# Performance work log

Measured on AMD Instinct MI355X. Metric: run time of the kernel, lower is better.

## Reference

```python
import jax, jax.numpy as jnp
import numpy as np

V = 23
EDGES = [(2,1),(3,1),(6,12),(6,10),(6,8),(8,10),(7,13),(7,11),(7,9),(9,11),(2,4),(4,6),(3,5),(5,7),(2,3),(2,14),(3,15),(14,15),(14,16),(15,17),(16,18),(17,19),(18,20),(18,22),(20,22),(19,21),(19,23),(21,23)]
K, H, C, OUT_C = 3, 8, 128, 128
N, T = 32, 256
BN_EPS = 1e-5


def _hop_matrix():
    # binarized union of I, Fw, Bw as in Graph.get_hop_distance
    A = np.zeros((V, V))
    for i, j in EDGES:
        A[i - 1, j - 1] = 1.0
        A[j - 1, i - 1] = 1.0
    np.fill_diagonal(A, 1.0)
    hop = np.full((V, V), V, dtype=np.int32)
    P = np.eye(V)
    for d in range(V):
        reach = P > 0
        hop = np.where(reach & (hop == V), d, hop)  # smallest d with reachability
        P = P @ A
    assert hop.max() < V, 'graph must be connected'
    return hop


def setup_inputs() -> dict:
    key = jax.random.key(0)
    ks = jax.random.split(key, 8)
    hop = _hop_matrix()  # (V,V) int32, max hop = 8 for mediapipe layout
    n_hop = int(hop.max()) + 1
    cin_g = C // H            # 16 in-channels per group
    cout_g = OUT_C // H       # 16 out-channels per group
    return {
        'x': jax.random.normal(ks[0], (N, C, T, V), dtype=jnp.float32),
        'emb_table': jax.random.normal(ks[1], (K, H, n_hop), dtype=jnp.float32) * 0.1,
        'A': jnp.tile(jnp.eye(V, dtype=jnp.float32)[None, None], (K, H, 1, 1))
             + 0.01 * jax.random.normal(ks[2], (K, H, V, V), dtype=jnp.float32),
        'conv_w': jax.random.normal(ks[3], (K * OUT_C, cin_g), dtype=jnp.float32) * 0.05,
        'conv_b': jax.random.normal(ks[4], (K * OUT_C,), dtype=jnp.float32) * 0.05,
        'bn_gamma': jax.random.uniform(ks[5], (OUT_C,), dtype=jnp.float32, minval=0.5, maxval=1.5),
        'bn_beta': jax.random.normal(ks[6], (OUT_C,), dtype=jnp.float32) * 0.1,
        'bn_mean': jax.random.normal(ks[7], (OUT_C,), dtype=jnp.float32) * 0.1,
        'bn_var': jax.random.uniform(jax.random.fold_in(key, 99), (OUT_C,), dtype=jnp.float32, minval=0.5, maxval=1.5),
        'hop': jnp.asarray(hop),
    }


def reference(x, emb_table, A, conv_w, conv_b, bn_gamma, bn_beta, bn_mean, bn_var, hop):
    n, c, t, v = x.shape
    k, h = A.shape[0], A.shape[1]
    cin_g = c // h
    # per-kernel/per-head learned adjacency from hop embedding table
    B = emb_table[:, :, hop]                                   # (k,h,v,v)
    def l2(w):
        return jnp.sqrt(jnp.sum(w * w, axis=-2, keepdims=True)) + 1e-4
    BnA = B / l2(B) + A / l2(A)                                # (k,h,v,v)
    xh = x.reshape(n, h, cin_g, t, v)
    # graph mixing over nodes (k-dim broadcast of x)
    y = jnp.einsum('nhctv,khvw->nkhctw', xh, BnA)              # (n,k,h,c/h,t,v)
    # grouped 1x1 conv (groups = k*h): per (k,h) group 16->16 channel mix
    w = conv_w.reshape(k, h, -1, cin_g)                        # (k,h,out/h,c/h)
    b = conv_b.reshape(k, h, -1)                               # (k,h,out/h)
    y = jnp.einsum('nkhctv,khoc->nkhotv', y, w) + b[None, :, :, :, None, None]
    y = y.reshape(n, k, -1, t, v).sum(axis=1)                  # (n,out_c,t,v)
    # BatchNorm2d (eval mode)
    inv = bn_gamma / jnp.sqrt(bn_var + BN_EPS)
    y = y * inv[None, :, None, None] + (bn_beta - bn_mean * inv)[None, :, None, None]
    # residual is identity (in_channels == out_channels)
    return jax.nn.relu(y + x)
```

## Files before the change

### kernel.cpp

```cpp
#include <hip/hip_runtime.h>
#include <hip/hip_bf16.h>
#include <stdint.h>

#define V 23
#define VP 24
#define KK 3
#define H 8
#define CG 16
#define TDIM 256
#define NB 32
#define TT 64
#define OUTC 128
#define CIN 128
#define KDIM 384
#define NSTEP 12
#define NCT 24
#define XROW 392

#define WS_BNA   0
#define WS_SCALE (KK*H*VP*VP)
#define WS_OFFS  (WS_SCALE + OUTC)
#define WS_WT    (WS_OFFS + OUTC)
#define WS_MB    (WS_WT + KK*H*CG*CG)
#define MB_ELEMS ((size_t)H * NSTEP * NCT * 512)
#define WS_NEED_BYTES ((size_t)WS_MB * 4 + MB_ELEMS * 2)
#define WS_SMALL_BYTES ((size_t)WS_MB * 4)

typedef __attribute__((ext_vector_type(8))) short bf16x8;
typedef __attribute__((ext_vector_type(4))) float f32x4;

static __device__ __forceinline__ uint32_t f2bf_rne(float f) {
  uint32_t u = __float_as_uint(f);
  return (u + 0x7fffu + ((u >> 16) & 1u)) >> 16;
}
static __device__ __forceinline__ float bf2f(uint16_t h) {
  return __uint_as_float(((uint32_t)h) << 16);
}

__global__ void prep1_kernel(const float* __restrict__ emb,
                             const float* __restrict__ A,
                             const float* __restrict__ conv_w,
                             const float* __restrict__ conv_b,
                             const float* __restrict__ gamma,
                             const float* __restrict__ beta,
                             const float* __restrict__ mean,
                             const float* __restrict__ var,
                             const int* __restrict__ hop,
                             int n_hop, float* __restrict__ ws) {
  int b = blockIdx.x;
  int tid = threadIdx.x;
  if (b < KK * H) {
    int w = tid;
    if (w >= 32) return;
    const float* e = emb + b * n_hop;
    const float* a = A + b * V * V;
    float nb = 1.f, na = 1.f;
    if (w < V) {
      float sb = 0.f, sa = 0.f;
      for (int v = 0; v < V; ++v) {
        float bv = e[hop[v * V + w]];
        float av = a[v * V + w];
        sb += bv * bv;
        sa += av * av;
      }
      nb = sqrtf(sb) + 1e-4f;
      na = sqrtf(sa) + 1e-4f;
    }
    float* dst = ws + WS_BNA + b * VP * VP;
    if (w < VP) {
      for (int v = 0; v < VP; ++v) {
        float val = 0.f;
        if (v < V && w < V)
          val = e[hop[v * V + w]] / nb + a[v * V + w] / na;
        dst[v * VP + w] = val;
      }
    }
  } else if (b == KK * H) {
    if (tid < OUTC) {
      float inv = gamma[tid] * rsqrtf(var[tid] + 1e-5f);
      float sb = conv_b[tid] + conv_b[OUTC + tid] + conv_b[2 * OUTC + tid];
      ws[WS_SCALE + tid] = inv;
      ws[WS_OFFS + tid] = beta[tid] - mean[tid] * inv + sb * inv;
    }
  } else {
    int idx = (b - KK * H - 1) * 256 + tid;
    if (idx < KK * H * CG * CG) {
      int o = idx & 15, c = (idx >> 4) & 15, h = (idx >> 8) & 7, k = idx >> 11;
      ws[WS_WT + ((k * H + h) * CG + c) * CG + o] =
          conv_w[((k * OUTC) + h * CG + o) * CG + c];
    }
  }
}

__global__ void prep2_kernel(float* __restrict__ ws) {
  int b = blockIdx.x;
  int h = b / NSTEP, s = b % NSTEP;
  uint16_t* mb = (uint16_t*)(ws + WS_MB);
  const float* wt = ws + WS_WT;
  const float* bna = ws + WS_BNA;
  for (int e = threadIdx.x; e < NCT * 64 * 8; e += 256) {
    int j = e & 7, lane = (e >> 3) & 63, ct = e >> 9;
    int k = s * 32 + ((lane >> 4) << 3) + j;
    int ci = k / VP, v = k % VP;
    int col = ct * 16 + (lane & 15);
    int o = col / VP, w = col - o * VP;
    float val = 0.f;
    if (v < V && w < V) {
      for (int kk = 0; kk < KK; ++kk)
        val += wt[((kk * H + h) * CG + ci) * CG + o] *
               bna[((kk * H + h) * VP + v) * VP + w];
    }
    mb[((size_t)(h * NSTEP + s) * NCT + ct) * 512 + lane * 8 + j] =
        (uint16_t)f2bf_rne(val);
  }
}

__global__ __launch_bounds__(256, 3) void gcn_main_mfma(
    const float* __restrict__ x,
    const float* __restrict__ ws,
    float* __restrict__ out) {
  __shared__ __align__(16) uint16_t Xa[TT * XROW];

  const int tid = threadIdx.x;
  const int t0 = blockIdx.x * TT;
  const int h  = blockIdx.y;
  const int n  = blockIdx.z;

  for (int u = tid; u < CG * TT * 6; u += 256) {
    int c = u / (TT * 6);
    int r = u % (TT * 6);
    int tt = r / 6, vc = r % 6;
    const float* xrow =
        x + ((size_t)((n * CIN + h * CG + c) * TDIM) + (t0 + tt)) * V;
    float f0 = xrow[vc * 4 + 0];
    float f1 = xrow[vc * 4 + 1];
    float f2 = xrow[vc * 4 + 2];
    float f3 = (vc < 5) ? xrow[vc * 4 + 3] : 0.f;
    uint32_t lo = f2bf_rne(f0) | (f2bf_rne(f1) << 16);
    uint32_t hi = f2bf_rne(f2) | (f2bf_rne(f3) << 16);
    *(uint2*)&Xa[tt * XROW + c * VP + vc * 4] = make_uint2(lo, hi);
  }
  __syncthreads();

  const int wave = tid >> 6, lane = tid & 63;
  const int m = lane & 15, q = lane >> 4;

  const uint16_t* mb = (const uint16_t*)(ws + WS_MB) +
                       ((size_t)h * NSTEP * NCT + wave * 6) * 512 + lane * 8;

  f32x4 acc[4][6];
#pragma unroll
  for (int rt = 0; rt < 4; ++rt)
#pragma unroll
    for (int c6 = 0; c6 < 6; ++c6) acc[rt][c6] = (f32x4){0.f, 0.f, 0.f, 0.f};

  for (int s = 0; s < NSTEP; ++s) {
    bf16x8 bf[6];
#pragma unroll
    for (int c6 = 0; c6 < 6; ++c6)
      bf[c6] = *(const bf16x8*)(mb + (size_t)(s * NCT + c6) * 512);
    bf16x8 af[4];
#pragma unroll
    for (int rt = 0; rt < 4; ++rt)
      af[rt] = *(const bf16x8*)&Xa[(rt * 16 + m) * XROW + s * 32 + q * 8];
#pragma unroll
    for (int c6 = 0; c6 < 6; ++c6)
#pragma unroll
      for (int rt = 0; rt < 4; ++rt)
        acc[rt][c6] = __builtin_amdgcn_mfma_f32_16x16x32_bf16(
            af[rt], bf[c6], acc[rt][c6], 0, 0, 0);
  }

#pragma unroll
  for (int c6 = 0; c6 < 6; ++c6) {
    int col = (wave * 6 + c6) * 16 + m;
    int o = col / VP, w = col - o * VP;
    float sc = ws[WS_SCALE + h * CG + o];
    float of = ws[WS_OFFS + h * CG + o];
    bool valid = (w < V);
    float* obase =
        out + ((size_t)(n * OUTC + h * CG + o) * TDIM + t0) * V + w;
#pragma unroll
    for (int rt = 0; rt < 4; ++rt) {
#pragma unroll
      for (int reg = 0; reg < 4; ++reg) {
        int row = rt * 16 + q * 4 + reg;
        float resid = bf2f(Xa[row * XROW + col]);
        float y = fmaf(acc[rt][c6][reg], sc, of) + resid;
        if (valid) obase[(size_t)row * V] = fmaxf(y, 0.f);
      }
    }
  }
}

__global__ __launch_bounds__(256, 3) void gcn_main_valu(
    const float* __restrict__ x,
    const float* __restrict__ ws,
    float* __restrict__ out) {
  __shared__ __align__(16) uint16_t Xs[CG * TT * VP];

  const int tid = threadIdx.x;
  const int t0 = blockIdx.x * TT;
  const int h  = blockIdx.y;
  const int n  = blockIdx.z;

  for (int u = tid; u < CG * TT * 6; u += 256) {
    int c = u / (TT * 6);
    int r = u % (TT * 6);
    int tt = r / 6, vc = r % 6;
    const float* xrow =
        x + ((size_t)((n * CIN + h * CG + c) * TDIM) + (t0 + tt)) * V;
    float f0 = xrow[vc * 4 + 0];
    float f1 = xrow[vc * 4 + 1];
    float f2 = xrow[vc * 4 + 2];
    float f3 = (vc < 5) ? xrow[vc * 4 + 3] : 0.f;
    uint32_t lo = f2bf_rne(f0) | (f2bf_rne(f1) << 16);
    uint32_t hi = f2bf_rne(f2) | (f2bf_rne(f3) << 16);
    *(uint2*)&Xs[(c * TT + tt) * VP + vc * 4] = make_uint2(lo, hi);
  }
  __syncthreads();

  const int oq = __builtin_amdgcn_readfirstlane(tid >> 6);
  const int tt = tid & 63;

  const float* wt  = ws + WS_WT  + ((size_t)h * CG * CG);
  const float* bna = ws + WS_BNA + ((size_t)h * VP * VP);

  float acc[4][VP];
#pragma unroll
  for (int o = 0; o < 4; ++o)
#pragma unroll
    for (int w = 0; w < VP; ++w) acc[o][w] = 0.f;

  for (int k = 0; k < KK; ++k) {
    const float* wtk  = wt  + (size_t)k * H * CG * CG;
    const float* bnak = bna + (size_t)k * H * VP * VP;
    for (int vb = 0; vb < 3; ++vb) {
      float xwv[4][8];
#pragma unroll
      for (int o = 0; o < 4; ++o)
#pragma unroll
        for (int j = 0; j < 8; ++j) xwv[o][j] = 0.f;
#pragma unroll 4
      for (int c = 0; c < CG; ++c) {
        uint4 raw = *(const uint4*)&Xs[(c * TT + tt) * VP + vb * 8];
        float4 wv = *(const float4*)&wtk[c * CG + (oq << 2)];
        float xv[8];
        xv[0] = __uint_as_float(raw.x << 16);
        xv[1] = __uint_as_float(raw.x & 0xffff0000u);
        xv[2] = __uint_as_float(raw.y << 16);
        xv[3] = __uint_as_float(raw.y & 0xffff0000u);
        xv[4] = __uint_as_float(raw.z << 16);
        xv[5] = __uint_as_float(raw.z & 0xffff0000u);
        xv[6] = __uint_as_float(raw.w << 16);
        xv[7] = __uint_as_float(raw.w & 0xffff0000u);
#pragma unroll
        for (int o = 0; o < 4; ++o) {
          float wo = (&wv.x)[o];
#pragma unroll
          for (int j = 0; j < 8; ++j) xwv[o][j] = fmaf(wo, xv[j], xwv[o][j]);
        }
      }
#pragma unroll
      for (int j = 0; j < 8; ++j) {
        const int v = vb * 8 + j;
        const float* bnrow = &bnak[v * VP];
#pragma unroll
        for (int wb = 0; wb < 6; ++wb) {
          float4 bn = *(const float4*)(bnrow + wb * 4);
#pragma unroll
          for (int o = 0; o < 4; ++o) {
            acc[o][wb * 4 + 0] = fmaf(xwv[o][j], bn.x, acc[o][wb * 4 + 0]);
            acc[o][wb * 4 + 1] = fmaf(xwv[o][j], bn.y, acc[o][wb * 4 + 1]);
            acc[o][wb * 4 + 2] = fmaf(xwv[o][j], bn.z, acc[o][wb * 4 + 2]);
            acc[o][wb * 4 + 3] = fmaf(xwv[o][j], bn.w, acc[o][wb * 4 + 3]);
          }
        }
      }
    }
  }

#pragma unroll
  for (int o = 0; o < 4; ++o) {
    int og = (oq << 2) + o;
    int oc = h * CG + og;
    float sc = ws[WS_SCALE + oc];
    float of = ws[WS_OFFS + oc];
    float* orow = out + ((size_t)(n * OUTC + oc) * TDIM + (t0 + tt)) * V;
    const uint16_t* xsrow = &Xs[(og * TT + tt) * VP];
#pragma unroll
    for (int w = 0; w < V; ++w) {
      float resid = bf2f(xsrow[w]);
      float y = fmaf(acc[o][w], sc, of) + resid;
      orow[w] = fmaxf(y, 0.f);
    }
  }
}

extern "C" void kernel_launch(void* const* d_in, const int* in_sizes, int n_in,
                              void* d_out, int out_size, void* d_ws, size_t ws_size,
                              hipStream_t stream) {
  const float* x      = (const float*)d_in[0];
  const float* emb    = (const float*)d_in[1];
  const float* A      = (const float*)d_in[2];
  const float* conv_w = (const float*)d_in[3];
  const float* conv_b = (const float*)d_in[4];
  const float* gamma  = (const float*)d_in[5];
  const float* beta   = (const float*)d_in[6];
  const float* mean   = (const float*)d_in[7];
  const float* var    = (const float*)d_in[8];
  const int*   hop    = (const int*)d_in[9];
  float* ws  = (float*)d_ws;
  float* out = (float*)d_out;

  int n_hop = in_sizes[1] / (KK * H);

  prep1_kernel<<<dim3(KK * H + 1 + 24), dim3(256), 0, stream>>>(
      emb, A, conv_w, conv_b, gamma, beta, mean, var, hop, n_hop, ws);

  if (ws_size >= WS_NEED_BYTES) {
    prep2_kernel<<<dim3(H * NSTEP), dim3(256), 0, stream>>>(ws);
    gcn_main_mfma<<<dim3(TDIM / TT, H, NB), dim3(256), 0, stream>>>(x, ws, out);
  } else {
    gcn_main_valu<<<dim3(TDIM / TT, H, NB), dim3(256), 0, stream>>>(x, ws, out);
  }
}
```

Baseline: 249.6 us.

## Halve main-kernel time tile and parallelize prep kernels across more blocks

```diff
diff --git a/kernel.cpp b/kernel.cpp
--- a/kernel.cpp
+++ b/kernel.cpp
@@ -10,6 +10,7 @@
 #define TDIM 256
 #define NB 32
 #define TT 64
+#define TTM 32
 #define OUTC 128
 #define CIN 128
 #define KDIM 384
@@ -50,30 +51,33 @@
   int b = blockIdx.x;
   int tid = threadIdx.x;
   if (b < KK * H) {
-    int w = tid;
-    if (w >= 32) return;
+    __shared__ float nbv[VP], nav[VP];
     const float* e = emb + b * n_hop;
     const float* a = A + b * V * V;
-    float nb = 1.f, na = 1.f;
-    if (w < V) {
-      float sb = 0.f, sa = 0.f;
-      for (int v = 0; v < V; ++v) {
-        float bv = e[hop[v * V + w]];
-        float av = a[v * V + w];
-        sb += bv * bv;
-        sa += av * av;
+    if (tid < VP) {
+      float nb = 1.f, na = 1.f;
+      if (tid < V) {
+        float sb = 0.f, sa = 0.f;
+        for (int v = 0; v < V; ++v) {
+          float bv = e[hop[v * V + tid]];
+          float av = a[v * V + tid];
+          sb += bv * bv;
+          sa += av * av;
+        }
+        nb = sqrtf(sb) + 1e-4f;
+        na = sqrtf(sa) + 1e-4f;
       }
-      nb = sqrtf(sb) + 1e-4f;
-      na = sqrtf(sa) + 1e-4f;
-    }
+      nbv[tid] = nb;
+      nav[tid] = na;
+    }
+    __syncthreads();
     float* dst = ws + WS_BNA + b * VP * VP;
-    if (w < VP) {
-      for (int v = 0; v < VP; ++v) {
-        float val = 0.f;
-        if (v < V && w < V)
-          val = e[hop[v * V + w]] / nb + a[v * V + w] / na;
-        dst[v * VP + w] = val;
-      }
+    for (int idx = tid; idx < VP * VP; idx += 256) {
+      int v = idx / VP, w = idx % VP;
+      float val = 0.f;
+      if (v < V && w < V)
+        val = e[hop[v * V + w]] / nbv[w] + a[v * V + w] / nav[w];
+      dst[idx] = val;
     }
   } else if (b == KK * H) {
     if (tid < OUTC) {
@@ -93,42 +97,53 @@
 }
 
 __global__ void prep2_kernel(float* __restrict__ ws) {
-  int b = blockIdx.x;
-  int h = b / NSTEP, s = b % NSTEP;
-  uint16_t* mb = (uint16_t*)(ws + WS_MB);
+  __shared__ float WtL[KK][CG * CG];
+  __shared__ float BnL[KK][VP * VP];
+  int hs = blockIdx.x;
+  int chunk = blockIdx.y;
+  int h = hs / NSTEP, s = hs % NSTEP;
   const float* wt = ws + WS_WT;
   const float* bna = ws + WS_BNA;
-  for (int e = threadIdx.x; e < NCT * 64 * 8; e += 256) {
-    int j = e & 7, lane = (e >> 3) & 63, ct = e >> 9;
+  for (int i = threadIdx.x; i < KK * CG * CG; i += 256) {
+    int kk = i / (CG * CG), rest = i % (CG * CG);
+    WtL[kk][rest] = wt[(kk * H + h) * CG * CG + rest];
+  }
+  for (int i = threadIdx.x; i < KK * VP * VP; i += 256) {
+    int kk = i / (VP * VP), rest = i % (VP * VP);
+    BnL[kk][rest] = bna[(kk * H + h) * VP * VP + rest];
+  }
+  __syncthreads();
+  uint16_t* mb = (uint16_t*)(ws + WS_MB);
+  for (int e = threadIdx.x; e < 6 * 64 * 8; e += 256) {
+    int j = e & 7, lane = (e >> 3) & 63, ct = chunk * 6 + (e >> 9);
     int k = s * 32 + ((lane >> 4) << 3) + j;
-    int ci = k / VP, v = k % VP;
+    int ci = k / VP, v = k - ci * VP;
     int col = ct * 16 + (lane & 15);
     int o = col / VP, w = col - o * VP;
     float val = 0.f;
     if (v < V && w < V) {
       for (int kk = 0; kk < KK; ++kk)
-        val += wt[((kk * H + h) * CG + ci) * CG + o] *
-               bna[((kk * H + h) * VP + v) * VP + w];
+        val += WtL[kk][ci * CG + o] * BnL[kk][v * VP + w];
     }
     mb[((size_t)(h * NSTEP + s) * NCT + ct) * 512 + lane * 8 + j] =
         (uint16_t)f2bf_rne(val);
   }
 }
 
-__global__ __launch_bounds__(256, 3) void gcn_main_mfma(
+__global__ __launch_bounds__(256, 4) void gcn_main_mfma(
     const float* __restrict__ x,
     const float* __restrict__ ws,
     float* __restrict__ out) {
-  __shared__ __align__(16) uint16_t Xa[TT * XROW];
+  __shared__ __align__(16) uint16_t Xa[TTM * XROW];
 
   const int tid = threadIdx.x;
-  const int t0 = blockIdx.x * TT;
+  const int t0 = blockIdx.x * TTM;
   const int h  = blockIdx.y;
   const int n  = blockIdx.z;
 
-  for (int u = tid; u < CG * TT * 6; u += 256) {
-    int c = u / (TT * 6);
-    int r = u % (TT * 6);
+  for (int u = tid; u < CG * TTM * 6; u += 256) {
+    int c = u / (TTM * 6);
+    int r = u % (TTM * 6);
     int tt = r / 6, vc = r % 6;
     const float* xrow =
         x + ((size_t)((n * CIN + h * CG + c) * TDIM) + (t0 + tt)) * V;
@@ -148,9 +163,9 @@
   const uint16_t* mb = (const uint16_t*)(ws + WS_MB) +
                        ((size_t)h * NSTEP * NCT + wave * 6) * 512 + lane * 8;
 
-  f32x4 acc[4][6];
-#pragma unroll
-  for (int rt = 0; rt < 4; ++rt)
+  f32x4 acc[2][6];
+#pragma unroll
+  for (int rt = 0; rt < 2; ++rt)
 #pragma unroll
     for (int c6 = 0; c6 < 6; ++c6) acc[rt][c6] = (f32x4){0.f, 0.f, 0.f, 0.f};
 
@@ -159,14 +174,14 @@
 #pragma unroll
     for (int c6 = 0; c6 < 6; ++c6)
       bf[c6] = *(const bf16x8*)(mb + (size_t)(s * NCT + c6) * 512);
-    bf16x8 af[4];
-#pragma unroll
-    for (int rt = 0; rt < 4; ++rt)
+    bf16x8 af[2];
+#pragma unroll
+    for (int rt = 0; rt < 2; ++rt)
       af[rt] = *(const bf16x8*)&Xa[(rt * 16 + m) * XROW + s * 32 + q * 8];
 #pragma unroll
     for (int c6 = 0; c6 < 6; ++c6)
 #pragma unroll
-      for (int rt = 0; rt < 4; ++rt)
+      for (int rt = 0; rt < 2; ++rt)
         acc[rt][c6] = __builtin_amdgcn_mfma_f32_16x16x32_bf16(
             af[rt], bf[c6], acc[rt][c6], 0, 0, 0);
   }
@@ -181,7 +196,7 @@
     float* obase =
         out + ((size_t)(n * OUTC + h * CG + o) * TDIM + t0) * V + w;
 #pragma unroll
-    for (int rt = 0; rt < 4; ++rt) {
+    for (int rt = 0; rt < 2; ++rt) {
 #pragma unroll
       for (int reg = 0; reg < 4; ++reg) {
         int row = rt * 16 + q * 4 + reg;
@@ -319,8 +334,8 @@
       emb, A, conv_w, conv_b, gamma, beta, mean, var, hop, n_hop, ws);
 
   if (ws_size >= WS_NEED_BYTES) {
-    prep2_kernel<<<dim3(H * NSTEP), dim3(256), 0, stream>>>(ws);
-    gcn_main_mfma<<<dim3(TDIM / TT, H, NB), dim3(256), 0, stream>>>(x, ws, out);
+    prep2_kernel<<<dim3(H * NSTEP, 4), dim3(256), 0, stream>>>(ws);
+    gcn_main_mfma<<<dim3(TDIM / TTM, H, NB), dim3(256), 0, stream>>>(x, ws, out);
   } else {
     gcn_main_valu<<<dim3(TDIM / TT, H, NB), dim3(256), 0, stream>>>(x, ws, out);
   }
```

Measured after the change: 238.5 us. -4.5%, faster.
